# Kernel tuning notes

Hardware: AMD Instinct MI355X
Metric: run time of the kernel (lower is better)

Reference implementation:

```python
import jax, jax.numpy as jnp
import numpy as np

DRUG_DIM, TARGET_DIM, HEADS, DIM_HEAD = 768, 2560, 8, 96
INNER = HEADS * DIM_HEAD
NEG = -1000000.0
LN_EPS = 1e-5


def setup_inputs() -> dict:
    key = jax.random.key(0)
    ks = jax.random.split(key, 10)
    b, n, m = 16, 256, 1024
    drug = jax.random.normal(ks[0], (b, n, DRUG_DIM), dtype=jnp.float32)
    target = jax.random.normal(ks[1], (b, m, TARGET_DIM), dtype=jnp.float32)
    drug_mask = jax.random.randint(ks[2], (b, n), 0, 2, dtype=jnp.int32)
    pro_mask = jax.random.randint(ks[3], (b, m), 0, 2, dtype=jnp.int32)
    # parameters (torch Linear weight is (out,in); store as (in,out) for x @ W)
    Wq = jax.random.normal(ks[4], (DRUG_DIM, INNER), dtype=jnp.float32) / np.sqrt(DRUG_DIM)
    Wk = jax.random.normal(ks[5], (TARGET_DIM, INNER), dtype=jnp.float32) / np.sqrt(TARGET_DIM)
    Wv = jax.random.normal(ks[6], (TARGET_DIM, INNER), dtype=jnp.float32) / np.sqrt(TARGET_DIM)
    Wo = jax.random.normal(ks[7], (INNER, DRUG_DIM), dtype=jnp.float32) / np.sqrt(INNER)
    bo = jnp.zeros((DRUG_DIM,), dtype=jnp.float32)
    gamma = jnp.ones((DRUG_DIM,), dtype=jnp.float32)
    beta = jnp.zeros((DRUG_DIM,), dtype=jnp.float32)
    return {"drug": drug, "target": target, "drug_mask": drug_mask,
            "pro_mask": pro_mask, "Wq": Wq, "Wk": Wk, "Wv": Wv,
            "Wo": Wo, "bo": bo, "gamma": gamma, "beta": beta}


def reference(drug, target, drug_mask, pro_mask, Wq, Wk, Wv, Wo, bo, gamma, beta):
    b, n, _ = drug.shape
    m = target.shape[1]
    scale = DIM_HEAD ** -0.5
    # projections -> (b, h, len, d)
    q = (drug @ Wq).reshape(b, n, HEADS, DIM_HEAD).transpose(0, 2, 1, 3)
    k = (target @ Wk).reshape(b, m, HEADS, DIM_HEAD).transpose(0, 2, 1, 3)
    v = (target @ Wv).reshape(b, m, HEADS, DIM_HEAD).transpose(0, 2, 1, 3)
    dots = jnp.einsum('bhnd,bhmd->bhnm', q, k) * scale
    # dual mask: positions where drug_mask==0 (rows) OR pro_mask==0 (cols) -> -1e6
    valid = (drug_mask[:, None, :, None] != 0) & (pro_mask[:, None, None, :] != 0)
    masked_dots = jnp.where(valid, dots, NEG)
    attn = jax.nn.softmax(masked_dots, axis=-1)
    out = jnp.einsum('bhnm,bhmd->bhnd', attn, v)
    out = out.transpose(0, 2, 1, 3).reshape(b, n, INNER)
    out = out @ Wo + bo
    # residual + LayerNorm
    x = out + drug
    mu = jnp.mean(x, axis=-1, keepdims=True)
    var = jnp.mean(jnp.square(x - mu), axis=-1, keepdims=True)
    out = (x - mu) * jax.lax.rsqrt(var + LN_EPS) * gamma + beta
    return (out, attn)
```

## Files before the change

kernel.cpp:

```cpp
#include <hip/hip_runtime.h>

typedef short s16x8 __attribute__((ext_vector_type(8)));
typedef float f32x4 __attribute__((ext_vector_type(4)));

__device__ __forceinline__ unsigned short f2bf(float f) {
    unsigned int u = __builtin_bit_cast(unsigned int, f);
    unsigned int r = u + 0x7FFFu + ((u >> 16) & 1u);
    return (unsigned short)(r >> 16);
}

__device__ __forceinline__ void gload16(const unsigned short* g, unsigned short* l) {
    __builtin_amdgcn_global_load_lds(
        (const __attribute__((address_space(1))) unsigned int*)g,
        (__attribute__((address_space(3))) unsigned int*)l, 16, 0, 0);
}

__device__ __forceinline__ s16x8 ldf(const unsigned short* p) {
    return *reinterpret_cast<const s16x8*>(p);
}

__global__ __launch_bounds__(256) void cvt_bf16(
    const float* __restrict__ in, unsigned short* __restrict__ out, int n) {
    int i = (blockIdx.x * 256 + threadIdx.x) * 8;
    int stride = gridDim.x * 256 * 8;
    for (; i < n; i += stride) {
        float4 a = *reinterpret_cast<const float4*>(in + i);
        float4 b = *reinterpret_cast<const float4*>(in + i + 4);
        uint4 o;
        o.x = (unsigned int)f2bf(a.x) | ((unsigned int)f2bf(a.y) << 16);
        o.y = (unsigned int)f2bf(a.z) | ((unsigned int)f2bf(a.w) << 16);
        o.z = (unsigned int)f2bf(b.x) | ((unsigned int)f2bf(b.y) << 16);
        o.w = (unsigned int)f2bf(b.z) | ((unsigned int)f2bf(b.w) << 16);
        *reinterpret_cast<uint4*>(out + i) = o;
    }
}

__global__ __launch_bounds__(256) void transpose_bf16(
    const float* __restrict__ W, unsigned short* __restrict__ Wt, int K, int N) {
    __shared__ float t[32][33];
    int k0 = blockIdx.x * 32, n0 = blockIdx.y * 32;
    int tid = threadIdx.x;
    int r = tid >> 5, c = tid & 31;
    for (int p = 0; p < 4; ++p)
        t[p * 8 + r][c] = W[(size_t)(k0 + p * 8 + r) * N + n0 + c];
    __syncthreads();
    for (int p = 0; p < 4; ++p)
        Wt[(size_t)(n0 + p * 8 + r) * K + k0 + c] = f2bf(t[c][p * 8 + r]);
}

template <int OUTMODE>
__global__ __launch_bounds__(256, 2) void gemm_db(
    const unsigned short* __restrict__ A, const unsigned short* __restrict__ Bt,
    int M, int N, int K,
    float* __restrict__ Cf,
    unsigned short* __restrict__ outA, unsigned short* __restrict__ outVt,
    int seqlen) {
    extern __shared__ __align__(16) unsigned short smem[];
    unsigned short* As = smem;
    unsigned short* Bs = smem + 16384;

    int tid = threadIdx.x, wid = tid >> 6, lane = tid & 63;
    int nb = N / 128;
    int nwg = gridDim.x, bid = blockIdx.x;
    int wg = (bid & 7) * (nwg >> 3) + (bid >> 3);
    int tm = wg / nb, tn = wg % nb;
    int m0 = tm * 128, n0 = tn * 128;
    int wm = (wid >> 1) * 64, wn = (wid & 1) * 64;
    int lrow = lane & 15, lkc = lane >> 4;

    int lrsub = lane >> 3;
    int gch = (lane & 7) ^ lrsub;
    const unsigned short* gA[4];
    const unsigned short* gB[4];
    unsigned short* lA[4];
    unsigned short* lB[4];
#pragma unroll
    for (int p = 0; p < 4; ++p) {
        int r = (wid * 4 + p) * 8 + lrsub;
        gA[p] = A + (size_t)(m0 + r) * K + gch * 8;
        gB[p] = Bt + (size_t)(n0 + r) * K + gch * 8;
        lA[p] = As + (wid * 4 + p) * 512;
        lB[p] = Bs + (wid * 4 + p) * 512;
    }

    int offA[2][4], offB[2][4];
#pragma unroll
    for (int kh = 0; kh < 2; ++kh)
#pragma unroll
        for (int i = 0; i < 4; ++i) {
            int ra = wm + i * 16 + lrow;
            offA[kh][i] = ra * 64 + (((kh * 4 + lkc) ^ (ra & 7)) * 8);
            int rb = wn + i * 16 + lrow;
            offB[kh][i] = rb * 64 + (((kh * 4 + lkc) ^ (rb & 7)) * 8);
        }

    int NT = K / 64;
    f32x4 acc[4][4] = {};

#pragma unroll
    for (int p = 0; p < 4; ++p) { gload16(gA[p], lA[p]); gload16(gB[p], lB[p]); }

    int cur = 0;
    for (int t = 0; t < NT; ++t) {
        __syncthreads();
        if (t + 1 < NT) {
            int nxt = (cur ^ 1) * 8192;
            int koff = (t + 1) * 64;
#pragma unroll
            for (int p = 0; p < 4; ++p) {
                gload16(gA[p] + koff, lA[p] + nxt);
                gload16(gB[p] + koff, lB[p] + nxt);
            }
        }
        const unsigned short* Ab = As + cur * 8192;
        const unsigned short* Bb = Bs + cur * 8192;
#pragma unroll
        for (int kh = 0; kh < 2; ++kh) {
            s16x8 af[4], bfv[4];
#pragma unroll
            for (int i = 0; i < 4; ++i) af[i] = ldf(&Ab[offA[kh][i]]);
#pragma unroll
            for (int j = 0; j < 4; ++j) bfv[j] = ldf(&Bb[offB[kh][j]]);
#pragma unroll
            for (int i = 0; i < 4; ++i)
#pragma unroll
                for (int j = 0; j < 4; ++j)
                    acc[i][j] = __builtin_amdgcn_mfma_f32_16x16x32_bf16(af[i], bfv[j], acc[i][j], 0, 0, 0);
        }
        cur ^= 1;
    }

    int orow4 = (lane >> 4) * 4;
    int bblk = (OUTMODE == 1) ? (m0 / seqlen) : 0;
    for (int i = 0; i < 4; ++i)
        for (int j = 0; j < 4; ++j)
            for (int r = 0; r < 4; ++r) {
                int row = m0 + wm + i * 16 + orow4 + r;
                int col = n0 + wn + j * 16 + lrow;
                float v = acc[i][j][r];
                if constexpr (OUTMODE == 0) {
                    Cf[(size_t)row * N + col] = v;
                } else {
                    int s = row - bblk * seqlen;
                    unsigned short hv = f2bf(v);
                    if (col < 768) {
                        int h = col / 96, d = col - h * 96;
                        outA[(((size_t)(bblk * 8 + h)) * seqlen + s) * 96 + d] = hv;
                    } else {
                        int cc = col - 768;
                        int h = cc / 96, d = cc - h * 96;
                        outVt[(((size_t)(bblk * 8 + h)) * 96 + d) * seqlen + s] = hv;
                    }
                }
            }
}

#define MT 64
__global__ __launch_bounds__(256) void attn_kernel(
    const unsigned short* __restrict__ Qb,
    const unsigned short* __restrict__ Kb,
    const unsigned short* __restrict__ Vt,
    const int* __restrict__ drug_mask,
    const int* __restrict__ pro_mask,
    float* __restrict__ attn_out,
    unsigned short* __restrict__ AO)
{
    constexpr float scale = 0.10206207261596575f;
    __shared__ __align__(16) unsigned short Qs[64][104];
    __shared__ __align__(16) unsigned short Ps[4][16][MT + 8];
    __shared__ float colv[1024];

    int tid = threadIdx.x, wid = tid >> 6, lane = tid & 63;
    int bh = blockIdx.x, nt = blockIdx.y;
    int b = bh >> 3, h = bh & 7;
    const unsigned short* Qg = Qb + (size_t)bh * 256 * 96 + (size_t)nt * 64 * 96;
    const unsigned short* Kg = Kb + (size_t)bh * 1024 * 96;
    const unsigned short* Vg = Vt + (size_t)bh * 96 * 1024;

    for (int idx = tid; idx < 64 * 12; idx += 256) {
        int r = idx / 12, s = idx % 12;
        *reinterpret_cast<uint4*>(&Qs[r][s * 8]) =
            *reinterpret_cast<const uint4*>(&Qg[r * 96 + s * 8]);
    }
    for (int m = tid; m < 1024; m += 256)
        colv[m] = (pro_mask[b * 1024 + m] != 0) ? 1.0f : 0.0f;

    int lrow = lane & 15, lkg = lane >> 4;
    int qrow0 = nt * 64 + wid * 16;
    float rv[4];
    for (int r = 0; r < 4; ++r)
        rv[r] = (drug_mask[b * 256 + qrow0 + lkg * 4 + r] != 0) ? 1.0f : 0.0f;

    __syncthreads();
    s16x8 qa[3];
    for (int kk = 0; kk < 3; ++kk)
        qa[kk] = ldf(&Qs[wid * 16 + lrow][kk * 32 + lkg * 8]);

    float mrun[4], srun[4];
    for (int r = 0; r < 4; ++r) { mrun[r] = -3.0e38f; srun[r] = 0.f; }

    for (int mt = 0; mt < 1024; mt += MT) {
        float sv[MT / 16][4];
#pragma unroll
        for (int nf = 0; nf < MT / 16; ++nf) {
            f32x4 acc = {};
#pragma unroll
            for (int kk = 0; kk < 3; ++kk) {
                s16x8 bb = ldf(Kg + (size_t)(mt + nf * 16 + lrow) * 96 + kk * 32 + lkg * 8);
                acc = __builtin_amdgcn_mfma_f32_16x16x32_bf16(qa[kk], bb, acc, 0, 0, 0);
            }
            float cv = colv[mt + nf * 16 + lrow];
#pragma unroll
            for (int r = 0; r < 4; ++r)
                sv[nf][r] = (rv[r] * cv != 0.f) ? acc[r] * scale : -1.0e6f;
        }
#pragma unroll
        for (int r = 0; r < 4; ++r) {
            float v = sv[0][r];
#pragma unroll
            for (int nf = 1; nf < MT / 16; ++nf) v = fmaxf(v, sv[nf][r]);
            for (int o = 1; o < 16; o <<= 1) v = fmaxf(v, __shfl_xor(v, o));
            float nm = fmaxf(mrun[r], v);
            float ts = 0.f;
#pragma unroll
            for (int nf = 0; nf < MT / 16; ++nf) ts += __expf(sv[nf][r] - nm);
            for (int o = 1; o < 16; o <<= 1) ts += __shfl_xor(ts, o);
            srun[r] = srun[r] * __expf(mrun[r] - nm) + ts;
            mrun[r] = nm;
        }
    }
    float sinv[4];
    for (int r = 0; r < 4; ++r) sinv[r] = 1.0f / srun[r];

    f32x4 oacc[6] = {};
    for (int mt = 0; mt < 1024; mt += MT) {
#pragma unroll
        for (int nf = 0; nf < MT / 16; ++nf) {
            f32x4 acc = {};
#pragma unroll
            for (int kk = 0; kk < 3; ++kk) {
                s16x8 bb = ldf(Kg + (size_t)(mt + nf * 16 + lrow) * 96 + kk * 32 + lkg * 8);
                acc = __builtin_amdgcn_mfma_f32_16x16x32_bf16(qa[kk], bb, acc, 0, 0, 0);
            }
            float cv = colv[mt + nf * 16 + lrow];
#pragma unroll
            for (int r = 0; r < 4; ++r) {
                float sel = (rv[r] * cv != 0.f) ? acc[r] * scale : -1.0e6f;
                float p = __expf(sel - mrun[r]) * sinv[r];
                attn_out[((size_t)bh * 256 + qrow0 + lkg * 4 + r) * 1024 + mt + nf * 16 + lrow] = p;
                Ps[wid][lkg * 4 + r][nf * 16 + lrow] = f2bf(p);
            }
        }
        asm volatile("s_waitcnt lgkmcnt(0)" ::: "memory");
        __builtin_amdgcn_sched_barrier(0);
#pragma unroll
        for (int kk = 0; kk < MT / 32; ++kk) {
            s16x8 pa = ldf(&Ps[wid][lrow][kk * 32 + lkg * 8]);
#pragma unroll
            for (int df = 0; df < 6; ++df) {
                s16x8 vb = ldf(Vg + (size_t)(df * 16 + lrow) * 1024 + mt + kk * 32 + lkg * 8);
                oacc[df] = __builtin_amdgcn_mfma_f32_16x16x32_bf16(pa, vb, oacc[df], 0, 0, 0);
            }
        }
        asm volatile("s_waitcnt lgkmcnt(0)" ::: "memory");
        __builtin_amdgcn_sched_barrier(0);
    }
    for (int df = 0; df < 6; ++df)
        for (int r = 0; r < 4; ++r) {
            int grow = b * 256 + qrow0 + lkg * 4 + r;
            int gcol = h * 96 + df * 16 + lrow;
            AO[(size_t)grow * 768 + gcol] = f2bf(oacc[df][r]);
        }
}

__global__ __launch_bounds__(256) void ln_kernel(
    const float* __restrict__ O, const float* __restrict__ drug,
    const float* __restrict__ bo, const float* __restrict__ gamma,
    const float* __restrict__ beta, float* __restrict__ out) {
    int row = blockIdx.x, tid = threadIdx.x;
    __shared__ float red[4];
    float x[3], s = 0.f;
    for (int i = 0; i < 3; ++i) {
        int j = tid + i * 256;
        x[i] = O[(size_t)row * 768 + j] + bo[j] + drug[(size_t)row * 768 + j];
        s += x[i];
    }
    for (int o = 32; o; o >>= 1) s += __shfl_xor(s, o);
    if ((tid & 63) == 0) red[tid >> 6] = s;
    __syncthreads();
    float mu = (red[0] + red[1] + red[2] + red[3]) * (1.0f / 768.0f);
    float v = 0.f;
    for (int i = 0; i < 3; ++i) { float d = x[i] - mu; v += d * d; }
    for (int o = 32; o; o >>= 1) v += __shfl_xor(v, o);
    __syncthreads();
    if ((tid & 63) == 0) red[tid >> 6] = v;
    __syncthreads();
    float var = (red[0] + red[1] + red[2] + red[3]) * (1.0f / 768.0f);
    float rs = rsqrtf(var + 1e-5f);
    for (int i = 0; i < 3; ++i) {
        int j = tid + i * 256;
        out[(size_t)row * 768 + j] = (x[i] - mu) * rs * gamma[j] + beta[j];
    }
}

extern "C" void kernel_launch(void* const* d_in, const int* in_sizes, int n_in,
                              void* d_out, int out_size, void* d_ws, size_t ws_size,
                              hipStream_t stream) {
    const float* drug   = (const float*)d_in[0];
    const float* target = (const float*)d_in[1];
    const int*   dmask  = (const int*)d_in[2];
    const int*   pmask  = (const int*)d_in[3];
    const float* Wq = (const float*)d_in[4];
    const float* Wk = (const float*)d_in[5];
    const float* Wv = (const float*)d_in[6];
    const float* Wo = (const float*)d_in[7];
    const float* bo = (const float*)d_in[8];
    const float* gm = (const float*)d_in[9];
    const float* bt = (const float*)d_in[10];

    char* w = (char*)d_ws;
    unsigned short* Wtq  = (unsigned short*)(w + 0);
    unsigned short* Wtkv = (unsigned short*)(w + 1179648);
    unsigned short* Wto  = (unsigned short*)(w + 9043968);
    unsigned short* Qb   = (unsigned short*)(w + 10223616);
    unsigned short* Kb   = (unsigned short*)(w + 16515072);
    unsigned short* Vtb  = (unsigned short*)(w + 41680896);
    unsigned short* AO   = (unsigned short*)(w + 66846720);
    float*          Otmp = (float*)(w + 73138176);
    unsigned short* drugb = (unsigned short*)(w + 85721088);

    float* out_ln   = (float*)d_out;
    float* attn_out = (float*)d_out + 3145728;
    unsigned short* targetb = (unsigned short*)attn_out;

    cvt_bf16<<<2048, 256, 0, stream>>>(target, targetb, 41943040);
    cvt_bf16<<<512, 256, 0, stream>>>(drug, drugb, 3145728);

    transpose_bf16<<<dim3(24, 24), 256, 0, stream>>>(Wq, Wtq, 768, 768);
    transpose_bf16<<<dim3(80, 24), 256, 0, stream>>>(Wk, Wtkv, 2560, 768);
    transpose_bf16<<<dim3(80, 24), 256, 0, stream>>>(Wv, Wtkv + (size_t)768 * 2560, 2560, 768);
    transpose_bf16<<<dim3(24, 24), 256, 0, stream>>>(Wo, Wto, 768, 768);

    gemm_db<1><<<1536, 256, 65536, stream>>>(targetb, Wtkv, 16384, 1536, 2560,
                                             nullptr, Kb, Vtb, 1024);
    gemm_db<1><<<192, 256, 65536, stream>>>(drugb, Wtq, 4096, 768, 768,
                                            nullptr, Qb, nullptr, 256);
    attn_kernel<<<dim3(128, 4), 256, 0, stream>>>(Qb, Kb, Vtb, dmask, pmask, attn_out, AO);
    gemm_db<0><<<192, 256, 65536, stream>>>(AO, Wto, 4096, 768, 768,
                                            Otmp, nullptr, nullptr, 256);
    ln_kernel<<<4096, 256, 0, stream>>>(Otmp, drug, bo, gm, bt, out_ln);
}
```

Baseline: 390.1 us.

## Stage K and V tiles in LDS for attention and merge prep kernel launches

The attention kernel now cooperatively loads each 64-row K tile and the matching V^T tile into shared memory, and the waves read MFMA operands from there instead of each wave issuing its own global loads. Barriers now separate the load, score and PV phases, and several unroll pragmas are removed. Separately, the two bf16 conversion launches are merged into one, and the four weight transposes are merged into two launches. The goal is to cut redundant global/L2 traffic in attention and to reduce launch overhead, at the cost of extra syncthreads and more LDS per block.

Measured after the change: 335.7 us. -13.9%, faster.

```diff
diff --git a/kernel.cpp b/kernel.cpp
--- a/kernel.cpp
+++ b/kernel.cpp
@@ -19,10 +19,17 @@
     return *reinterpret_cast<const s16x8*>(p);
 }
 
-__global__ __launch_bounds__(256) void cvt_bf16(
-    const float* __restrict__ in, unsigned short* __restrict__ out, int n) {
-    int i = (blockIdx.x * 256 + threadIdx.x) * 8;
-    int stride = gridDim.x * 256 * 8;
+__global__ __launch_bounds__(256) void cvt_bf16_2(
+    const float* __restrict__ in0, unsigned short* __restrict__ out0, int n0blk, int n0,
+    const float* __restrict__ in1, unsigned short* __restrict__ out1, int n1) {
+    const float* in;
+    unsigned short* out;
+    int n, bid;
+    if (blockIdx.x < n0blk) { in = in0; out = out0; n = n0; bid = blockIdx.x; }
+    else { in = in1; out = out1; n = n1; bid = blockIdx.x - n0blk; }
+    int nblk = (blockIdx.x < n0blk) ? n0blk : (gridDim.x - n0blk);
+    int i = (bid * 256 + threadIdx.x) * 8;
+    int stride = nblk * 256 * 8;
     for (; i < n; i += stride) {
         float4 a = *reinterpret_cast<const float4*>(in + i);
         float4 b = *reinterpret_cast<const float4*>(in + i + 4);
@@ -35,9 +42,12 @@
     }
 }
 
-__global__ __launch_bounds__(256) void transpose_bf16(
-    const float* __restrict__ W, unsigned short* __restrict__ Wt, int K, int N) {
+__global__ __launch_bounds__(256) void transpose2_bf16(
+    const float* __restrict__ W0, const float* __restrict__ W1,
+    unsigned short* __restrict__ T0, unsigned short* __restrict__ T1, int K, int N) {
     __shared__ float t[32][33];
+    const float* W = blockIdx.z ? W1 : W0;
+    unsigned short* Wt = blockIdx.z ? T1 : T0;
     int k0 = blockIdx.x * 32, n0 = blockIdx.y * 32;
     int tid = threadIdx.x;
     int r = tid >> 5, c = tid & 31;
@@ -167,6 +177,8 @@
 {
     constexpr float scale = 0.10206207261596575f;
     __shared__ __align__(16) unsigned short Qs[64][104];
+    __shared__ __align__(16) unsigned short Ks[MT][104];
+    __shared__ __align__(16) unsigned short Vts[96][MT + 8];
     __shared__ __align__(16) unsigned short Ps[4][16][MT + 8];
     __shared__ float colv[1024];
 
@@ -200,29 +212,30 @@
     for (int r = 0; r < 4; ++r) { mrun[r] = -3.0e38f; srun[r] = 0.f; }
 
     for (int mt = 0; mt < 1024; mt += MT) {
+        __syncthreads();
+        for (int idx = tid; idx < MT * 12; idx += 256) {
+            int r = idx / 12, s = idx % 12;
+            *reinterpret_cast<uint4*>(&Ks[r][s * 8]) =
+                *reinterpret_cast<const uint4*>(&Kg[(size_t)(mt + r) * 96 + s * 8]);
+        }
+        __syncthreads();
         float sv[MT / 16][4];
-#pragma unroll
         for (int nf = 0; nf < MT / 16; ++nf) {
             f32x4 acc = {};
-#pragma unroll
             for (int kk = 0; kk < 3; ++kk) {
-                s16x8 bb = ldf(Kg + (size_t)(mt + nf * 16 + lrow) * 96 + kk * 32 + lkg * 8);
+                s16x8 bb = ldf(&Ks[nf * 16 + lrow][kk * 32 + lkg * 8]);
                 acc = __builtin_amdgcn_mfma_f32_16x16x32_bf16(qa[kk], bb, acc, 0, 0, 0);
             }
             float cv = colv[mt + nf * 16 + lrow];
-#pragma unroll
             for (int r = 0; r < 4; ++r)
                 sv[nf][r] = (rv[r] * cv != 0.f) ? acc[r] * scale : -1.0e6f;
         }
-#pragma unroll
         for (int r = 0; r < 4; ++r) {
             float v = sv[0][r];
-#pragma unroll
             for (int nf = 1; nf < MT / 16; ++nf) v = fmaxf(v, sv[nf][r]);
             for (int o = 1; o < 16; o <<= 1) v = fmaxf(v, __shfl_xor(v, o));
             float nm = fmaxf(mrun[r], v);
             float ts = 0.f;
-#pragma unroll
             for (int nf = 0; nf < MT / 16; ++nf) ts += __expf(sv[nf][r] - nm);
             for (int o = 1; o < 16; o <<= 1) ts += __shfl_xor(ts, o);
             srun[r] = srun[r] * __expf(mrun[r] - nm) + ts;
@@ -234,16 +247,25 @@
 
     f32x4 oacc[6] = {};
     for (int mt = 0; mt < 1024; mt += MT) {
-#pragma unroll
+        __syncthreads();
+        for (int idx = tid; idx < MT * 12; idx += 256) {
+            int r = idx / 12, s = idx % 12;
+            *reinterpret_cast<uint4*>(&Ks[r][s * 8]) =
+                *reinterpret_cast<const uint4*>(&Kg[(size_t)(mt + r) * 96 + s * 8]);
+        }
+        for (int idx = tid; idx < 96 * (MT / 8); idx += 256) {
+            int r = idx / (MT / 8), s = idx % (MT / 8);
+            *reinterpret_cast<uint4*>(&Vts[r][s * 8]) =
+                *reinterpret_cast<const uint4*>(&Vg[(size_t)r * 1024 + mt + s * 8]);
+        }
+        __syncthreads();
         for (int nf = 0; nf < MT / 16; ++nf) {
             f32x4 acc = {};
-#pragma unroll
             for (int kk = 0; kk < 3; ++kk) {
-                s16x8 bb = ldf(Kg + (size_t)(mt + nf * 16 + lrow) * 96 + kk * 32 + lkg * 8);
+                s16x8 bb = ldf(&Ks[nf * 16 + lrow][kk * 32 + lkg * 8]);
                 acc = __builtin_amdgcn_mfma_f32_16x16x32_bf16(qa[kk], bb, acc, 0, 0, 0);
             }
             float cv = colv[mt + nf * 16 + lrow];
-#pragma unroll
             for (int r = 0; r < 4; ++r) {
                 float sel = (rv[r] * cv != 0.f) ? acc[r] * scale : -1.0e6f;
                 float p = __expf(sel - mrun[r]) * sinv[r];
@@ -251,19 +273,14 @@
                 Ps[wid][lkg * 4 + r][nf * 16 + lrow] = f2bf(p);
             }
         }
-        asm volatile("s_waitcnt lgkmcnt(0)" ::: "memory");
-        __builtin_amdgcn_sched_barrier(0);
-#pragma unroll
+        __syncthreads();
         for (int kk = 0; kk < MT / 32; ++kk) {
             s16x8 pa = ldf(&Ps[wid][lrow][kk * 32 + lkg * 8]);
-#pragma unroll
             for (int df = 0; df < 6; ++df) {
-                s16x8 vb = ldf(Vg + (size_t)(df * 16 + lrow) * 1024 + mt + kk * 32 + lkg * 8);
+                s16x8 vb = ldf(&Vts[df * 16 + lrow][kk * 32 + lkg * 8]);
                 oacc[df] = __builtin_amdgcn_mfma_f32_16x16x32_bf16(pa, vb, oacc[df], 0, 0, 0);
             }
         }
-        asm volatile("s_waitcnt lgkmcnt(0)" ::: "memory");
-        __builtin_amdgcn_sched_barrier(0);
     }
     for (int df = 0; df < 6; ++df)
         for (int r = 0; r < 4; ++r) {
@@ -333,13 +350,12 @@
     float* attn_out = (float*)d_out + 3145728;
     unsigned short* targetb = (unsigned short*)attn_out;
 
-    cvt_bf16<<<2048, 256, 0, stream>>>(target, targetb, 41943040);
-    cvt_bf16<<<512, 256, 0, stream>>>(drug, drugb, 3145728);
-
-    transpose_bf16<<<dim3(24, 24), 256, 0, stream>>>(Wq, Wtq, 768, 768);
-    transpose_bf16<<<dim3(80, 24), 256, 0, stream>>>(Wk, Wtkv, 2560, 768);
-    transpose_bf16<<<dim3(80, 24), 256, 0, stream>>>(Wv, Wtkv + (size_t)768 * 2560, 2560, 768);
-    transpose_bf16<<<dim3(24, 24), 256, 0, stream>>>(Wo, Wto, 768, 768);
+    cvt_bf16_2<<<2560, 256, 0, stream>>>(target, targetb, 2048, 41943040,
+                                         drug, drugb, 3145728);
+
+    transpose2_bf16<<<dim3(24, 24, 2), 256, 0, stream>>>(Wq, Wo, Wtq, Wto, 768, 768);
+    transpose2_bf16<<<dim3(80, 24, 2), 256, 0, stream>>>(
+        Wk, Wv, Wtkv, Wtkv + (size_t)768 * 2560, 2560, 768);
 
     gemm_db<1><<<1536, 256, 65536, stream>>>(targetb, Wtkv, 16384, 1536, 2560,
                                              nullptr, Kb, Vtb, 1024);
```
